# Kernel tuning notes

Measured on AMD Instinct MI355X. Metric: run time of the kernel, lower is better.

## Reference

```python
import jax, jax.numpy as jnp
import numpy as np

B, N, C, H, W = 2, 2048, 1024, 16, 8  # batch, seq, dim, heads, band half-width
HD = C // H
SCALE = HD ** -0.5


def band_mask(n, w):
    # rows i: allowed cols lo..hi inclusive, matching get_attn_mask
    i = jnp.arange(n)[:, None]
    j = jnp.arange(n)[None, :]
    lo = jnp.where(i <= w, 0, i - w)
    hi = jnp.where(n - i <= w, n - 1, i + w)
    return (j >= lo) & (j <= hi)  # [N, N] bool


def setup_inputs() -> dict:
    key = jax.random.key(0)
    k1, k2, k3 = jax.random.split(key, 3)
    x = jax.random.normal(k1, (B, N, C), dtype=jnp.float32)
    Wqkv = jax.random.normal(k2, (C, 3 * C), dtype=jnp.float32) * (C ** -0.5)
    Wproj = jax.random.normal(k3, (C, C), dtype=jnp.float32) * (C ** -0.5)
    bproj = jnp.zeros((C,), dtype=jnp.float32)
    return {"x": x, "Wqkv": Wqkv, "Wproj": Wproj, "bproj": bproj}


def reference(x, Wqkv, Wproj, bproj):
    b, n, c = x.shape
    qkv = (x @ Wqkv).reshape(b, n, 3, H, HD)
    qkv = jnp.transpose(qkv, (2, 0, 3, 1, 4))  # [3, B, H, N, HD]
    q, k, v = qkv[0], qkv[1], qkv[2]
    attn = jnp.einsum('bhqd,bhkd->bhqk', q, k) * SCALE
    mask = band_mask(n, W)  # [N, N]
    attn = jnp.where(mask[None, None], attn, jnp.float32(-1e9))
    attn = jax.nn.softmax(attn, axis=-1)
    # dropout omitted (eval mode / deterministic reference)
    out = jnp.einsum('bhqk,bhkd->bhqd', attn, v)
    out = jnp.transpose(out, (0, 2, 1, 3)).reshape(b, n, c)
    return out @ Wproj + bproj
```

## Files before the change

### kernel.cpp

```cpp
#include <hip/hip_runtime.h>

typedef unsigned short ushort_t;
typedef unsigned int uint32;

typedef __bf16 bf16x8 __attribute__((ext_vector_type(8)));
typedef float f32x4 __attribute__((ext_vector_type(4)));

#define BAR() __builtin_amdgcn_s_barrier()
#define LGKM0() asm volatile("s_waitcnt lgkmcnt(0)")
#define VMCNT(n) asm volatile("s_waitcnt vmcnt(" #n ")")

__device__ __forceinline__ uint32 f2bf1(float f) {
  uint32 b = __float_as_uint(f);
  return (b + 0x7FFFu + ((b >> 16) & 1u)) >> 16;
}
__device__ __forceinline__ uint32 packbf2(float a, float b) {
  return f2bf1(a) | (f2bf1(b) << 16);
}
__device__ __forceinline__ float bflo(uint32 u) { return __uint_as_float(u << 16); }
__device__ __forceinline__ float bfhi(uint32 u) { return __uint_as_float(u & 0xFFFF0000u); }

__device__ __forceinline__ void gload16(const void* g, void* l) {
  __builtin_amdgcn_global_load_lds(
      (const __attribute__((address_space(1))) unsigned int*)g,
      (__attribute__((address_space(3))) unsigned int*)l, 16, 0, 0);
}

__global__ __launch_bounds__(256) void cvt_f32_bf16(
    const float* __restrict__ in, ushort_t* __restrict__ out, int n4) {
  int i = blockIdx.x * 256 + threadIdx.x;
  if (i < n4) {
    float4 v = ((const float4*)in)[i];
    uint2 r;
    r.x = packbf2(v.x, v.y);
    r.y = packbf2(v.z, v.w);
    ((uint2*)out)[i] = r;
  }
}

__global__ __launch_bounds__(256) void transpose_cvt2(
    const float* __restrict__ Wqkv, ushort_t* __restrict__ wqkvT,
    const float* __restrict__ Wproj, ushort_t* __restrict__ wprT) {
  __shared__ float tile[32][33];
  const int tx = threadIdx.x & 31, ty = threadIdx.x >> 5;
  const int bx = blockIdx.x;
  const float* src;
  ushort_t* dst;
  int Cc, c0;
  if (bx < 96) { src = Wqkv; dst = wqkvT; Cc = 3072; c0 = bx << 5; }
  else         { src = Wproj; dst = wprT; Cc = 1024; c0 = (bx - 96) << 5; }
  const int r0 = blockIdx.y << 5;
#pragma unroll
  for (int i = 0; i < 4; ++i)
    tile[ty + i * 8][tx] = src[(size_t)(r0 + ty + i * 8) * Cc + c0 + tx];
  __syncthreads();
#pragma unroll
  for (int i = 0; i < 4; ++i)
    dst[(size_t)(c0 + ty + i * 8) * 1024 + r0 + tx] = (ushort_t)f2bf1(tile[tx][ty + i * 8]);
}


__device__ __forceinline__ void stage_half(ushort_t* ldsr, const ushort_t* g,
                                           int ldK, int tid) {
  const int r = tid >> 3, s = tid & 7;
  const int c = ((s ^ (r & 7)) << 3);
  const int wvb = (tid >> 6) << 9;
  gload16(g + (size_t)r * ldK + c, ldsr + wvb);
  gload16(g + (size_t)(r + 64) * ldK + c, ldsr + 4096 + wvb);
}

#define READ_A(qm_)                                             \
  {                                                             \
    const int ab = pA + (qm_) * 4096;                           \
    a_k0[0] = *(const bf16x8*)&lds[ab + cK0];                   \
    a_k1[0] = *(const bf16x8*)&lds[ab + cK1];                   \
    a_k0[1] = *(const bf16x8*)&lds[ab + 1024 + cK0];            \
    a_k1[1] = *(const bf16x8*)&lds[ab + 1024 + cK1];            \
    a_k0[2] = *(const bf16x8*)&lds[ab + 2048 + cK0];            \
    a_k1[2] = *(const bf16x8*)&lds[ab + 2048 + cK1];            \
    a_k0[3] = *(const bf16x8*)&lds[ab + 3072 + cK0];            \
    a_k1[3] = *(const bf16x8*)&lds[ab + 3072 + cK1];            \
  }

#define READ_B(bk0, bk1, qn_)                                   \
  {                                                             \
    const int bb = pB + (qn_) * 2048;                           \
    bk0[0] = *(const bf16x8*)&lds[bb + cK0];                    \
    bk1[0] = *(const bf16x8*)&lds[bb + cK1];                    \
    bk0[1] = *(const bf16x8*)&lds[bb + 1024 + cK0];             \
    bk1[1] = *(const bf16x8*)&lds[bb + 1024 + cK1];             \
  }

#define MFMAQ(qm_, qn_, bk0, bk1)                                              \
  {                                                                            \
    _Pragma("unroll") for (int m = 0; m < 4; ++m) {                            \
      acc[(qm_) * 4 + m][(qn_) * 2 + 0] = __builtin_amdgcn_mfma_f32_16x16x32_bf16( \
          a_k0[m], bk0[0], acc[(qm_) * 4 + m][(qn_) * 2 + 0], 0, 0, 0);        \
      acc[(qm_) * 4 + m][(qn_) * 2 + 0] = __builtin_amdgcn_mfma_f32_16x16x32_bf16( \
          a_k1[m], bk1[0], acc[(qm_) * 4 + m][(qn_) * 2 + 0], 0, 0, 0);        \
      acc[(qm_) * 4 + m][(qn_) * 2 + 1] = __builtin_amdgcn_mfma_f32_16x16x32_bf16( \
          a_k0[m], bk0[1], acc[(qm_) * 4 + m][(qn_) * 2 + 1], 0, 0, 0);        \
      acc[(qm_) * 4 + m][(qn_) * 2 + 1] = __builtin_amdgcn_mfma_f32_16x16x32_bf16( \
          a_k1[m], bk1[1], acc[(qm_) * 4 + m][(qn_) * 2 + 1], 0, 0, 0);        \
    }                                                                          \
  }

__global__ __launch_bounds__(512, 2) void gemm8p_bt(
    const ushort_t* __restrict__ A, const ushort_t* __restrict__ Bt,
    ushort_t* __restrict__ C, const int M, const int Nn, const int K) {
  __shared__ ushort_t lds[65536];
  const int tid = threadIdx.x;
  const int lane = tid & 63, wave = tid >> 6;
  const int wm = wave >> 2, wn = wave & 3;

  const int q8 = gridDim.x >> 3;
  const int wg = (blockIdx.x & 7) * q8 + (blockIdx.x >> 3);
  const int nbn = Nn >> 8;
  const int bm = (wg / nbn) << 8;
  const int bn = (wg % nbn) << 8;
  const int nt = K >> 6;

  const int l15 = lane & 15, l16 = lane >> 4, l7 = l15 & 7;
  const int cK0 = ((l16 ^ l7) << 3);
  const int cK1 = (((4 + l16) ^ l7) << 3);

  f32x4 acc[8][4] = {};
  bf16x8 a_k0[4], a_k1[4], b0_k0[2], b0_k1[2], b1_k0[2], b1_k1[2];

  stage_half(&lds[0], A + (size_t)bm * K, K, tid);
  stage_half(&lds[8192], A + (size_t)(bm + 128) * K, K, tid);
  stage_half(&lds[16384], Bt + (size_t)bn * K, K, tid);
  stage_half(&lds[16384 + 8192], Bt + (size_t)(bn + 128) * K, K, tid);
  stage_half(&lds[32768 + 16384], Bt + (size_t)bn * K + 64, K, tid);
  stage_half(&lds[32768 + 16384 + 8192], Bt + (size_t)(bn + 128) * K + 64, K, tid);
  VMCNT(4);
  BAR();

  for (int U = 0; U < nt; ++U) {
    const int p = U & 1;
    const int pA = p * 32768 + wm * 8192 + l15 * 64;
    const int pB = p * 32768 + 16384 + (wn >> 1) * 8192 + ((wn & 1) * 64 + l15) * 64;
    const bool sA = (U + 1) < nt;
    const bool sB = (U + 2) < nt;

    READ_A(0);
    READ_B(b0_k0, b0_k1, 0);
    if (sA) stage_half(&lds[(p ^ 1) * 32768], A + (size_t)bm * K + (U + 1) * 64, K, tid);
    BAR();
    LGKM0();
    __builtin_amdgcn_s_setprio(1);
    MFMAQ(0, 0, b0_k0, b0_k1);
    __builtin_amdgcn_s_setprio(0);
    BAR();

    READ_B(b1_k0, b1_k1, 1);
    if (sA) stage_half(&lds[(p ^ 1) * 32768 + 8192], A + (size_t)(bm + 128) * K + (U + 1) * 64, K, tid);
    BAR();
    LGKM0();
    __builtin_amdgcn_s_setprio(1);
    MFMAQ(0, 1, b1_k0, b1_k1);
    __builtin_amdgcn_s_setprio(0);
    BAR();

    READ_A(1);
    if (sB) stage_half(&lds[p * 32768 + 16384], Bt + (size_t)bn * K + (U + 2) * 64, K, tid);
    BAR();
    LGKM0();
    __builtin_amdgcn_s_setprio(1);
    MFMAQ(1, 1, b1_k0, b1_k1);
    __builtin_amdgcn_s_setprio(0);
    BAR();

    if (sB) stage_half(&lds[p * 32768 + 16384 + 8192], Bt + (size_t)(bn + 128) * K + (U + 2) * 64, K, tid);
    BAR();
    __builtin_amdgcn_s_setprio(1);
    MFMAQ(1, 0, b0_k0, b0_k1);
    __builtin_amdgcn_s_setprio(0);
    if (sB) {
      VMCNT(4);
    } else {
      VMCNT(0);
    }
    BAR();
  }

  const int crow0 = bm + wm * 128 + (l16 << 2);
  const int ccol0 = bn + wn * 64 + l15;
#pragma unroll
  for (int m = 0; m < 8; ++m)
#pragma unroll
    for (int n = 0; n < 4; ++n)
#pragma unroll
      for (int j = 0; j < 4; ++j)
        C[(size_t)(crow0 + m * 16 + j) * Nn + ccol0 + n * 16] =
            (ushort_t)f2bf1(acc[m][n][j]);
}

template <bool OUT_BF16>
__global__ __launch_bounds__(256) void gemm_bt(
    const ushort_t* __restrict__ A, const ushort_t* __restrict__ Bt,
    void* __restrict__ Cout, const float* __restrict__ bias,
    const int M, const int Nn, const int K) {
  __shared__ ushort_t lA[128 * 32];
  __shared__ ushort_t lB[128 * 32];
  const int tid = threadIdx.x;
  const int lane = tid & 63, wave = tid >> 6;
  const int wm = wave >> 1, wn = wave & 1;
  const int bm = blockIdx.y << 7, bn = blockIdx.x << 7;

  f32x4 acc[4][4] = {};

  const int srow = tid >> 2, schk = tid & 3;
  const ushort_t* gA = A + (size_t)(bm + srow) * K + schk * 8;
  const ushort_t* gB = Bt + (size_t)(bn + srow) * K + schk * 8;
  ushort_t* lA0 = lA + wave * 512;
  ushort_t* lB0 = lB + wave * 512;

  const int la_off = ((wm << 6) + (lane & 15)) * 32 + ((lane >> 4) << 3);
  const int lb_off = ((wn << 6) + (lane & 15)) * 32 + ((lane >> 4) << 3);

  for (int k0 = 0; k0 < K; k0 += 32) {
    gload16(gA + k0, lA0);
    gload16(gA + k0 + 64 * K, lA0 + 2048);
    gload16(gB + k0, lB0);
    gload16(gB + k0 + 64 * K, lB0 + 2048);
    __syncthreads();
    bf16x8 a[4], b[4];
#pragma unroll
    for (int m = 0; m < 4; ++m) a[m] = *(const bf16x8*)&lA[la_off + m * 512];
#pragma unroll
    for (int n = 0; n < 4; ++n) b[n] = *(const bf16x8*)&lB[lb_off + n * 512];
#pragma unroll
    for (int m = 0; m < 4; ++m)
#pragma unroll
      for (int n = 0; n < 4; ++n)
        acc[m][n] = __builtin_amdgcn_mfma_f32_16x16x32_bf16(a[m], b[n], acc[m][n], 0, 0, 0);
    __syncthreads();
  }

  const int r0 = bm + (wm << 6) + ((lane >> 4) << 2);
  const int c0 = bn + (wn << 6) + (lane & 15);
#pragma unroll
  for (int m = 0; m < 4; ++m)
#pragma unroll
    for (int n = 0; n < 4; ++n)
#pragma unroll
      for (int j = 0; j < 4; ++j) {
        const int row = r0 + m * 16 + j;
        const int col = c0 + n * 16;
        if (OUT_BF16)
          ((ushort_t*)Cout)[(size_t)row * Nn + col] = (ushort_t)f2bf1(acc[m][n][j]);
        else
          ((float*)Cout)[(size_t)row * Nn + col] = acc[m][n][j] + bias[col];
      }
}

__global__ __launch_bounds__(256) void attn_band(
    const ushort_t* __restrict__ qkv, ushort_t* __restrict__ aout) {
  __shared__ float Ks[80 * 68];
  __shared__ float Vs[80 * 68];
  const int tid = threadIdx.x;
  const int i0 = blockIdx.x << 6;
  const int h = blockIdx.y;
  const int b = blockIdx.z;
  const size_t rowbase = (size_t)b * 2048;

  for (int idx = tid; idx < 1280; idx += 256) {
    const int t = idx >> 4, c = idx & 15;
    const int j = i0 - 8 + t;
    float k0 = 0.f, k1 = 0.f, k2 = 0.f, k3 = 0.f;
    float v0 = 0.f, v1 = 0.f, v2 = 0.f, v3 = 0.f;
    if ((unsigned)j < 2048u) {
      const ushort_t* p = qkv + (rowbase + j) * 3072 + (h << 6) + (c << 2);
      uint2 rk = *(const uint2*)(p + 1024);
      uint2 rv = *(const uint2*)(p + 2048);
      k0 = bflo(rk.x); k1 = bfhi(rk.x); k2 = bflo(rk.y); k3 = bfhi(rk.y);
      v0 = bflo(rv.x); v1 = bfhi(rv.x); v2 = bflo(rv.y); v3 = bfhi(rv.y);
    }
    *(float4*)&Ks[t * 68 + (c << 2)] = make_float4(k0, k1, k2, k3);
    *(float4*)&Vs[t * 68 + (c << 2)] = make_float4(v0, v1, v2, v3);
  }
  __syncthreads();

  const int lane = tid & 63, wv = tid >> 6;
  const int qs = lane >> 2, dg = lane & 3;
  const int qi = (wv << 4) + qs;
  const int i = i0 + qi;

  const ushort_t* qp = qkv + (rowbase + i) * 3072 + (h << 6) + (dg << 4);
  float q[16];
  {
    uint4 u0 = *(const uint4*)qp;
    uint4 u1 = *(const uint4*)(qp + 8);
    q[0] = bflo(u0.x); q[1] = bfhi(u0.x); q[2] = bflo(u0.y); q[3] = bfhi(u0.y);
    q[4] = bflo(u0.z); q[5] = bfhi(u0.z); q[6] = bflo(u0.w); q[7] = bfhi(u0.w);
    q[8] = bflo(u1.x); q[9] = bfhi(u1.x); q[10] = bflo(u1.y); q[11] = bfhi(u1.y);
    q[12] = bflo(u1.z); q[13] = bfhi(u1.z); q[14] = bflo(u1.w); q[15] = bfhi(u1.w);
  }

  float s[17];
#pragma unroll
  for (int jo = 0; jo < 17; ++jo) {
    const float* kr = &Ks[(qi + jo) * 68 + (dg << 4)];
    float d = 0.f;
#pragma unroll
    for (int c = 0; c < 4; ++c) {
      float4 kv = *(const float4*)(kr + (c << 2));
      d += q[c * 4 + 0] * kv.x + q[c * 4 + 1] * kv.y +
           q[c * 4 + 2] * kv.z + q[c * 4 + 3] * kv.w;
    }
    d += __shfl_xor(d, 1);
    d += __shfl_xor(d, 2);
    const int jg = i - 8 + jo;
    s[jo] = ((unsigned)jg < 2048u) ? d * 0.125f : -1e30f;
  }
  float m = s[0];
#pragma unroll
  for (int jo = 1; jo < 17; ++jo) m = fmaxf(m, s[jo]);
  float sum = 0.f;
#pragma unroll
  for (int jo = 0; jo < 17; ++jo) {
    s[jo] = __expf(s[jo] - m);
    sum += s[jo];
  }
  const float inv = 1.f / sum;

  float o[16];
#pragma unroll
  for (int dd = 0; dd < 16; ++dd) o[dd] = 0.f;
#pragma unroll
  for (int jo = 0; jo < 17; ++jo) {
    const float* vr = &Vs[(qi + jo) * 68 + (dg << 4)];
    const float w = s[jo];
#pragma unroll
    for (int c = 0; c < 4; ++c) {
      float4 vv = *(const float4*)(vr + (c << 2));
      o[c * 4 + 0] += w * vv.x; o[c * 4 + 1] += w * vv.y;
      o[c * 4 + 2] += w * vv.z; o[c * 4 + 3] += w * vv.w;
    }
  }

  ushort_t* op = aout + (rowbase + i) * 1024 + (h << 6) + (dg << 4);
  uint4 w0, w1;
  w0.x = packbf2(o[0] * inv, o[1] * inv);
  w0.y = packbf2(o[2] * inv, o[3] * inv);
  w0.z = packbf2(o[4] * inv, o[5] * inv);
  w0.w = packbf2(o[6] * inv, o[7] * inv);
  w1.x = packbf2(o[8] * inv, o[9] * inv);
  w1.y = packbf2(o[10] * inv, o[11] * inv);
  w1.z = packbf2(o[12] * inv, o[13] * inv);
  w1.w = packbf2(o[14] * inv, o[15] * inv);
  *(uint4*)op = w0;
  *(uint4*)(op + 8) = w1;
}

extern "C" void kernel_launch(void* const* d_in, const int* in_sizes, int n_in,
                              void* d_out, int out_size, void* d_ws, size_t ws_size,
                              hipStream_t stream) {
  const float* x = (const float*)d_in[0];
  const float* Wqkv = (const float*)d_in[1];
  const float* Wproj = (const float*)d_in[2];
  const float* bproj = (const float*)d_in[3];
  float* out = (float*)d_out;

  char* ws = (char*)d_ws;
  ushort_t* xb    = (ushort_t*)(ws);
  ushort_t* wqkvT = (ushort_t*)(ws + (8u << 20));
  ushort_t* wprT  = (ushort_t*)(ws + (14u << 20));
  ushort_t* qkv   = (ushort_t*)(ws + (16u << 20));
  ushort_t* aoutb = (ushort_t*)(ws + (40u << 20));

  cvt_f32_bf16<<<4096, 256, 0, stream>>>(x, xb, 1048576);
  transpose_cvt2<<<dim3(128, 32), 256, 0, stream>>>(Wqkv, wqkvT, Wproj, wprT);
  gemm8p_bt<<<192, 512, 0, stream>>>(xb, wqkvT, qkv, 4096, 3072, 1024);
  attn_band<<<dim3(32, 16, 2), 256, 0, stream>>>(qkv, aoutb);
  gemm_bt<false><<<dim3(8, 32), 256, 0, stream>>>(aoutb, wprT, out, bproj, 4096, 1024, 1024);
}
```

Before: 92.61 us.

## Merge input prep kernels and unroll QKV GEMM loop by two stages

Folds the x conversion and weight transpose-convert into one launch, removing a kernel launch and its gap. The QKV GEMM main loop is manually unrolled over both LDS ping-pong buffers, so buffer offsets become compile-time constants. LDS reads now go through inline-asm ds_read_b128 with sched_barrier after the lgkmcnt wait, which pins instruction order. The occupancy hint on launch_bounds is dropped. These changes aim to cut launch overhead and address arithmetic, but they tie the schedule to the hand-written order and hide it from the compiler.

After: 105.8 us. +14.2%, slower.

```diff
diff --git a/kernel.cpp b/kernel.cpp
--- a/kernel.cpp
+++ b/kernel.cpp
@@ -7,7 +7,7 @@
 typedef float f32x4 __attribute__((ext_vector_type(4)));
 
 #define BAR() __builtin_amdgcn_s_barrier()
-#define LGKM0() asm volatile("s_waitcnt lgkmcnt(0)")
+#define LGKM0() do { asm volatile("s_waitcnt lgkmcnt(0)"); __builtin_amdgcn_sched_barrier(0); } while (0)
 #define VMCNT(n) asm volatile("s_waitcnt vmcnt(" #n ")")
 
 __device__ __forceinline__ uint32 f2bf1(float f) {
@@ -26,30 +26,37 @@
       (__attribute__((address_space(3))) unsigned int*)l, 16, 0, 0);
 }
 
-__global__ __launch_bounds__(256) void cvt_f32_bf16(
-    const float* __restrict__ in, ushort_t* __restrict__ out, int n4) {
-  int i = blockIdx.x * 256 + threadIdx.x;
-  if (i < n4) {
-    float4 v = ((const float4*)in)[i];
+__device__ __forceinline__ bf16x8 dsr16(unsigned byteaddr) {
+  bf16x8 r;
+  asm volatile("ds_read_b128 %0, %1" : "=v"(r) : "v"(byteaddr));
+  return r;
+}
+
+__global__ __launch_bounds__(256) void prep_inputs(
+    const float* __restrict__ x, ushort_t* __restrict__ xb,
+    const float* __restrict__ Wqkv, ushort_t* __restrict__ wqkvT,
+    const float* __restrict__ Wproj, ushort_t* __restrict__ wprT) {
+  int bx = blockIdx.x;
+  const int tid = threadIdx.x;
+  if (bx < 4096) {
+    const int i = bx * 256 + tid;
+    float4 v = ((const float4*)x)[i];
     uint2 r;
     r.x = packbf2(v.x, v.y);
     r.y = packbf2(v.z, v.w);
-    ((uint2*)out)[i] = r;
-  }
-}
-
-__global__ __launch_bounds__(256) void transpose_cvt2(
-    const float* __restrict__ Wqkv, ushort_t* __restrict__ wqkvT,
-    const float* __restrict__ Wproj, ushort_t* __restrict__ wprT) {
+    ((uint2*)xb)[i] = r;
+    return;
+  }
+  bx -= 4096;
+  const int gx = bx & 127, gy = bx >> 7;
   __shared__ float tile[32][33];
-  const int tx = threadIdx.x & 31, ty = threadIdx.x >> 5;
-  const int bx = blockIdx.x;
+  const int tx = tid & 31, ty = tid >> 5;
   const float* src;
   ushort_t* dst;
   int Cc, c0;
-  if (bx < 96) { src = Wqkv; dst = wqkvT; Cc = 3072; c0 = bx << 5; }
-  else         { src = Wproj; dst = wprT; Cc = 1024; c0 = (bx - 96) << 5; }
-  const int r0 = blockIdx.y << 5;
+  if (gx < 96) { src = Wqkv;  dst = wqkvT; Cc = 3072; c0 = gx << 5; }
+  else         { src = Wproj; dst = wprT;  Cc = 1024; c0 = (gx - 96) << 5; }
+  const int r0 = gy << 5;
 #pragma unroll
   for (int i = 0; i < 4; ++i)
     tile[ty + i * 8][tx] = src[(size_t)(r0 + ty + i * 8) * Cc + c0 + tx];
@@ -69,26 +76,26 @@
   gload16(g + (size_t)(r + 64) * ldK + c, ldsr + 4096 + wvb);
 }
 
-#define READ_A(qm_)                                             \
+#define READ_A(base_, qm_)                                      \
   {                                                             \
-    const int ab = pA + (qm_) * 4096;                           \
-    a_k0[0] = *(const bf16x8*)&lds[ab + cK0];                   \
-    a_k1[0] = *(const bf16x8*)&lds[ab + cK1];                   \
-    a_k0[1] = *(const bf16x8*)&lds[ab + 1024 + cK0];            \
-    a_k1[1] = *(const bf16x8*)&lds[ab + 1024 + cK1];            \
-    a_k0[2] = *(const bf16x8*)&lds[ab + 2048 + cK0];            \
-    a_k1[2] = *(const bf16x8*)&lds[ab + 2048 + cK1];            \
-    a_k0[3] = *(const bf16x8*)&lds[ab + 3072 + cK0];            \
-    a_k1[3] = *(const bf16x8*)&lds[ab + 3072 + cK1];            \
-  }
-
-#define READ_B(bk0, bk1, qn_)                                   \
+    const unsigned ab = lb + 2u * (unsigned)((base_) + pA + (qm_) * 4096); \
+    a_k0[0] = dsr16(ab + 2 * cK0);                              \
+    a_k1[0] = dsr16(ab + 2 * cK1);                              \
+    a_k0[1] = dsr16(ab + 2048 + 2 * cK0);                       \
+    a_k1[1] = dsr16(ab + 2048 + 2 * cK1);                       \
+    a_k0[2] = dsr16(ab + 4096 + 2 * cK0);                       \
+    a_k1[2] = dsr16(ab + 4096 + 2 * cK1);                       \
+    a_k0[3] = dsr16(ab + 6144 + 2 * cK0);                       \
+    a_k1[3] = dsr16(ab + 6144 + 2 * cK1);                       \
+  }
+
+#define READ_B(base_, bk0, bk1, qn_)                            \
   {                                                             \
-    const int bb = pB + (qn_) * 2048;                           \
-    bk0[0] = *(const bf16x8*)&lds[bb + cK0];                    \
-    bk1[0] = *(const bf16x8*)&lds[bb + cK1];                    \
-    bk0[1] = *(const bf16x8*)&lds[bb + 1024 + cK0];             \
-    bk1[1] = *(const bf16x8*)&lds[bb + 1024 + cK1];             \
+    const unsigned bb = lb + 2u * (unsigned)((base_) + pB + (qn_) * 2048); \
+    bk0[0] = dsr16(bb + 2 * cK0);                               \
+    bk1[0] = dsr16(bb + 2 * cK1);                               \
+    bk0[1] = dsr16(bb + 2048 + 2 * cK0);                        \
+    bk1[1] = dsr16(bb + 2048 + 2 * cK1);                        \
   }
 
 #define MFMAQ(qm_, qn_, bk0, bk1)                                              \
@@ -105,7 +112,10 @@
     }                                                                          \
   }
 
-__global__ __launch_bounds__(512, 2) void gemm8p_bt(
+#define PRIO1() __builtin_amdgcn_s_setprio(1)
+#define PRIO0() __builtin_amdgcn_s_setprio(0)
+
+__global__ __launch_bounds__(512) void gemm8p_bt(
     const ushort_t* __restrict__ A, const ushort_t* __restrict__ Bt,
     ushort_t* __restrict__ C, const int M, const int Nn, const int K) {
   __shared__ ushort_t lds[65536];
@@ -123,64 +133,80 @@
   const int l15 = lane & 15, l16 = lane >> 4, l7 = l15 & 7;
   const int cK0 = ((l16 ^ l7) << 3);
   const int cK1 = (((4 + l16) ^ l7) << 3);
+  const int pA = wm * 8192 + l15 * 64;
+  const int pB = 16384 + (wn >> 1) * 8192 + ((wn & 1) * 64 + l15) * 64;
+  const unsigned lb = (unsigned)(uintptr_t)&lds[0];
+
+  const ushort_t* gA0 = A + (size_t)bm * K;
+  const ushort_t* gA1 = A + (size_t)(bm + 128) * K;
+  const ushort_t* gB0 = Bt + (size_t)bn * K;
+  const ushort_t* gB1 = Bt + (size_t)(bn + 128) * K;
 
   f32x4 acc[8][4] = {};
   bf16x8 a_k0[4], a_k1[4], b0_k0[2], b0_k1[2], b1_k0[2], b1_k1[2];
 
-  stage_half(&lds[0], A + (size_t)bm * K, K, tid);
-  stage_half(&lds[8192], A + (size_t)(bm + 128) * K, K, tid);
-  stage_half(&lds[16384], Bt + (size_t)bn * K, K, tid);
-  stage_half(&lds[16384 + 8192], Bt + (size_t)(bn + 128) * K, K, tid);
-  stage_half(&lds[32768 + 16384], Bt + (size_t)bn * K + 64, K, tid);
-  stage_half(&lds[32768 + 16384 + 8192], Bt + (size_t)(bn + 128) * K + 64, K, tid);
+  stage_half(&lds[0],             gA0, K, tid);
+  stage_half(&lds[8192],          gA1, K, tid);
+  stage_half(&lds[16384],         gB0, K, tid);
+  stage_half(&lds[24576],         gB1, K, tid);
+  stage_half(&lds[32768 + 16384], gB0 + 64, K, tid);
+  stage_half(&lds[32768 + 24576], gB1 + 64, K, tid);
   VMCNT(4);
   BAR();
 
-  for (int U = 0; U < nt; ++U) {
-    const int p = U & 1;
-    const int pA = p * 32768 + wm * 8192 + l15 * 64;
-    const int pB = p * 32768 + 16384 + (wn >> 1) * 8192 + ((wn & 1) * 64 + l15) * 64;
-    const bool sA = (U + 1) < nt;
-    const bool sB = (U + 2) < nt;
-
-    READ_A(0);
-    READ_B(b0_k0, b0_k1, 0);
-    if (sA) stage_half(&lds[(p ^ 1) * 32768], A + (size_t)bm * K + (U + 1) * 64, K, tid);
-    BAR();
-    LGKM0();
-    __builtin_amdgcn_s_setprio(1);
-    MFMAQ(0, 0, b0_k0, b0_k1);
-    __builtin_amdgcn_s_setprio(0);
-    BAR();
-
-    READ_B(b1_k0, b1_k1, 1);
-    if (sA) stage_half(&lds[(p ^ 1) * 32768 + 8192], A + (size_t)(bm + 128) * K + (U + 1) * 64, K, tid);
-    BAR();
-    LGKM0();
-    __builtin_amdgcn_s_setprio(1);
-    MFMAQ(0, 1, b1_k0, b1_k1);
-    __builtin_amdgcn_s_setprio(0);
-    BAR();
-
-    READ_A(1);
-    if (sB) stage_half(&lds[p * 32768 + 16384], Bt + (size_t)bn * K + (U + 2) * 64, K, tid);
-    BAR();
-    LGKM0();
-    __builtin_amdgcn_s_setprio(1);
-    MFMAQ(1, 1, b1_k0, b1_k1);
-    __builtin_amdgcn_s_setprio(0);
-    BAR();
-
-    if (sB) stage_half(&lds[p * 32768 + 16384 + 8192], Bt + (size_t)(bn + 128) * K + (U + 2) * 64, K, tid);
-    BAR();
-    __builtin_amdgcn_s_setprio(1);
-    MFMAQ(1, 0, b0_k0, b0_k1);
-    __builtin_amdgcn_s_setprio(0);
-    if (sB) {
-      VMCNT(4);
-    } else {
-      VMCNT(0);
-    }
+  for (int u = 0; u < (nt >> 1); ++u) {
+    const int t = u << 1;
+    const bool s2 = (t + 2) < nt;
+    const int kc1 = (t + 1) << 6, kc2 = (t + 2) << 6, kc3 = (t + 3) << 6;
+
+    READ_A(0, 0);
+    READ_B(0, b0_k0, b0_k1, 0);
+    stage_half(&lds[32768], gA0 + kc1, K, tid);
+    BAR(); LGKM0();
+    PRIO1(); MFMAQ(0, 0, b0_k0, b0_k1); PRIO0();
+    BAR();
+
+    READ_B(0, b1_k0, b1_k1, 1);
+    stage_half(&lds[32768 + 8192], gA1 + kc1, K, tid);
+    BAR(); LGKM0();
+    PRIO1(); MFMAQ(0, 1, b1_k0, b1_k1); PRIO0();
+    BAR();
+
+    READ_A(0, 1);
+    if (s2) stage_half(&lds[16384], gB0 + kc2, K, tid);
+    BAR(); LGKM0();
+    PRIO1(); MFMAQ(1, 1, b1_k0, b1_k1); PRIO0();
+    BAR();
+
+    if (s2) stage_half(&lds[24576], gB1 + kc2, K, tid);
+    BAR();
+    PRIO1(); MFMAQ(1, 0, b0_k0, b0_k1); PRIO0();
+    if (s2) { VMCNT(4); } else { VMCNT(0); }
+    BAR();
+
+    READ_A(32768, 0);
+    READ_B(32768, b0_k0, b0_k1, 0);
+    if (s2) stage_half(&lds[0], gA0 + kc2, K, tid);
+    BAR(); LGKM0();
+    PRIO1(); MFMAQ(0, 0, b0_k0, b0_k1); PRIO0();
+    BAR();
+
+    READ_B(32768, b1_k0, b1_k1, 1);
+    if (s2) stage_half(&lds[8192], gA1 + kc2, K, tid);
+    BAR(); LGKM0();
+    PRIO1(); MFMAQ(0, 1, b1_k0, b1_k1); PRIO0();
+    BAR();
+
+    READ_A(32768, 1);
+    if (s2) stage_half(&lds[32768 + 16384], gB0 + kc3, K, tid);
+    BAR(); LGKM0();
+    PRIO1(); MFMAQ(1, 1, b1_k0, b1_k1); PRIO0();
+    BAR();
+
+    if (s2) stage_half(&lds[32768 + 24576], gB1 + kc3, K, tid);
+    BAR();
+    PRIO1(); MFMAQ(1, 0, b0_k0, b0_k1); PRIO0();
+    if (s2) { VMCNT(4); }
     BAR();
   }
 
@@ -370,8 +396,7 @@
   ushort_t* qkv   = (ushort_t*)(ws + (16u << 20));
   ushort_t* aoutb = (ushort_t*)(ws + (40u << 20));
 
-  cvt_f32_bf16<<<4096, 256, 0, stream>>>(x, xb, 1048576);
-  transpose_cvt2<<<dim3(128, 32), 256, 0, stream>>>(Wqkv, wqkvT, Wproj, wprT);
+  prep_inputs<<<8192, 256, 0, stream>>>(x, xb, Wqkv, wqkvT, Wproj, wprT);
   gemm8p_bt<<<192, 512, 0, stream>>>(xb, wqkvT, qkv, 4096, 3072, 1024);
   attn_band<<<dim3(32, 16, 2), 256, 0, stream>>>(qkv, aoutb);
   gemm_bt<false><<<dim3(8, 32), 256, 0, stream>>>(aoutb, wprT, out, bproj, 4096, 1024, 1024);
```
